# Kernel optimization log

Hardware: AMD Instinct MI355X
Metric: run time of the kernel (lower is better)

The kernel has to match this reference:

```python
import jax, jax.numpy as jnp
import numpy as np

B, L, D = 32, 512, 128
H, D0, D2 = 8, 32, 32
SIGMA = 1.0
NEG = -10000.0


def setup_inputs() -> dict:
    key = jax.random.key(0)
    k_x, k_m, k1, k2, k3, k_w = jax.random.split(key, 6)
    X = jax.random.normal(k_x, (B, L, D), dtype=jnp.float32)
    # random padding mask; guarantee at least one valid item per row
    mask = jax.random.uniform(k_m, (B, L)) < 0.9
    mask = mask.at[:, 0].set(True)
    # nn.Linear(d, H*d0, bias=False): weight shape [H*d0, d], y = x @ W^T
    W1 = SIGMA * jax.random.normal(k1, (H * D0, D), dtype=jnp.float32)
    W2 = SIGMA * jax.random.normal(k2, (H * D0, D), dtype=jnp.float32)
    W3 = SIGMA * jax.random.normal(k3, (H * D2, D), dtype=jnp.float32)
    w = SIGMA * jax.random.normal(k_w, (H, D2), dtype=jnp.float32)
    return {"X": X, "mask": mask, "W1": W1, "W2": W2, "W3": W3, "w": w}


def reference(X, mask, W1, W2, W3, w):
    b, l, d = X.shape
    h, d2 = w.shape
    d0 = W1.shape[0] // h
    Q = (X @ W1.T).reshape(b, l, h, d0)
    K = (X @ W2.T).reshape(b, l, h, d0)
    V = (X @ W3.T).reshape(b, l, h, d2)
    # scores: [B, H, L, L]
    scores = jnp.einsum('blhd,bmhd->bhlm', Q, K) / jnp.sqrt(jnp.asarray(d0, X.dtype))
    # outer-product symmetric pad mask [B,1,L,L]
    am = (mask[:, None, None, :] & mask[:, None, :, None])
    scores = jnp.where(am, scores, jnp.asarray(NEG, X.dtype))
    attn = jax.nn.softmax(scores, axis=-1)
    out = jnp.einsum('bhlm,bmhd->blhd', attn, V)  # [B,L,H,D2]
    v = jnp.einsum('blhd,hd->bl', out, w) / jnp.sqrt(jnp.asarray(h, X.dtype))
    v = jnp.where(mask, v, jnp.asarray(NEG, X.dtype))
    probs = jax.nn.softmax(v, axis=-1)
    return probs
```

## Files before the change

### kernel.cpp

```cpp
#include <hip/hip_runtime.h>
#include <hip/hip_bf16.h>


typedef __attribute__((ext_vector_type(8))) short bf16x8;
typedef __attribute__((ext_vector_type(4))) float f32x4;
typedef __attribute__((ext_vector_type(8))) unsigned short ushort8;
typedef __attribute__((ext_vector_type(4))) unsigned short ushort4v;

#define NEG (-10000.0f)
#define LOG2E 1.4426950408889634f
#define QSCALE (0.17677669529663687f * LOG2E)

__device__ __forceinline__ unsigned short bf16_rn(float x, float* rep) {
  unsigned u = __float_as_uint(x);
  unsigned r = (u + 0x7FFFu + ((u >> 16) & 1u)) >> 16;
  *rep = __uint_as_float(r << 16);
  return (unsigned short)r;
}

__global__ __launch_bounds__(256) void convert_kernel(
    const float* __restrict__ X, const float* __restrict__ W1,
    const float* __restrict__ W2, const float* __restrict__ W3,
    const float* __restrict__ w,
    unsigned short* __restrict__ X2, unsigned short* __restrict__ Wc) {
  const int bx = blockIdx.x, t = threadIdx.x;
  if (bx < 1056) {
    const float* src;
    unsigned short* dst;
    int row, c;
    if (bx < 1024) {
      const size_t flat = (size_t)bx * 2048 + t * 8;
      row = (int)(flat >> 7); c = (int)(flat & 127);
      src = &X[flat];
      dst = &X2[(size_t)row * 256 + c];
    } else {
      const int flat = (bx - 1024) * 2048 + t * 8;
      row = flat >> 7; c = flat & 127;
      src = (row < 256) ? &W1[(size_t)row * 128 + c]
                        : &W2[(size_t)(row - 256) * 128 + c];
      dst = &Wc[(size_t)row * 256 + c];
    }
    float xv[8];
    *(float4*)&xv[0] = *(const float4*)src;
    *(float4*)&xv[4] = *(const float4*)(src + 4);
    ushort8 hi, lo;
#pragma unroll
    for (int i = 0; i < 8; ++i) {
      float hf, lf;
      hi[i] = bf16_rn(xv[i], &hf);
      lo[i] = bf16_rn(xv[i] - hf, &lf);
    }
    *(ushort8*)dst = hi;
    *(ushort8*)(dst + 128) = lo;
  } else {
    __shared__ float uS[8][128];
    if (t < 128) {
#pragma unroll
      for (int h = 0; h < 8; ++h) {
        float acc = 0.f;
#pragma unroll
        for (int d = 0; d < 32; ++d)
          acc += W3[(h * 32 + d) * 128 + t] * w[h * 32 + d];
        uS[h][t] = acc * 0.3535533905932738f;
      }
    }
    __syncthreads();
    {
      const int r = t >> 5, c = (t & 31) * 4;
      float4 v = *(float4*)&uS[r][c];
      float vv[4] = {v.x, v.y, v.z, v.w};
      ushort4v hi, lo;
#pragma unroll
      for (int i = 0; i < 4; ++i) {
        float hf, lf;
        hi[i] = bf16_rn(vv[i], &hf);
        lo[i] = bf16_rn(vv[i] - hf, &lf);
      }
      *(ushort4v*)&Wc[(size_t)(512 + r) * 256 + c] = hi;
      *(ushort4v*)&Wc[(size_t)(512 + r) * 256 + 128 + c] = lo;
    }
    const ushort8 z = {};
    for (int i = t; i < 1792; i += 256)
      *(ushort8*)&Wc[(size_t)520 * 256 + i * 8] = z;
  }
}

__global__ __launch_bounds__(256) void proj_kernel(
    const unsigned short* __restrict__ X2, const unsigned short* __restrict__ Wc,
    unsigned short* __restrict__ Q2, unsigned short* __restrict__ K2,
    float* __restrict__ Vw) {
  __shared__ unsigned short XS[64][72], WSd[64][72], WSx[64][72];
  const int t = threadIdx.x;
  const int row0 = blockIdx.x * 64, col0 = blockIdx.y * 64;
  const int w = t >> 6, lane = t & 63, g = lane >> 4, r16 = lane & 15;
  const int srow = t >> 2, su = (t & 3) * 16;

  f32x4 acc[4];
#pragma unroll
  for (int n = 0; n < 4; ++n) acc[n] = (f32x4){0.f, 0.f, 0.f, 0.f};

  for (int kc = 0; kc < 256; kc += 64) {
    const int kcx = (kc + 128) & 255;
    if (kc) __syncthreads();
    {
      const size_t xo = (size_t)(row0 + srow) * 256 + kc + su;
      const size_t wd = (size_t)(col0 + srow) * 256 + kc + su;
      const size_t wx = (size_t)(col0 + srow) * 256 + kcx + su;
      ushort8 a = *(const ushort8*)&X2[xo];
      ushort8 b = *(const ushort8*)&X2[xo + 8];
      ushort8 c = *(const ushort8*)&Wc[wd];
      ushort8 d = *(const ushort8*)&Wc[wd + 8];
      ushort8 e = *(const ushort8*)&Wc[wx];
      ushort8 f = *(const ushort8*)&Wc[wx + 8];
      *(ushort8*)&XS[srow][su] = a;
      *(ushort8*)&XS[srow][su + 8] = b;
      *(ushort8*)&WSd[srow][su] = c;
      *(ushort8*)&WSd[srow][su + 8] = d;
      *(ushort8*)&WSx[srow][su] = e;
      *(ushort8*)&WSx[srow][su + 8] = f;
    }
    __syncthreads();
#pragma unroll
    for (int ks = 0; ks < 2; ++ks) {
      bf16x8 ah = *(const bf16x8*)&XS[w * 16 + r16][ks * 32 + g * 8];
#pragma unroll
      for (int n = 0; n < 4; ++n) {
        bf16x8 bd = *(const bf16x8*)&WSd[n * 16 + r16][ks * 32 + g * 8];
        bf16x8 bx = *(const bf16x8*)&WSx[n * 16 + r16][ks * 32 + g * 8];
        acc[n] = __builtin_amdgcn_mfma_f32_16x16x32_bf16(ah, bd, acc[n], 0, 0, 0);
        acc[n] = __builtin_amdgcn_mfma_f32_16x16x32_bf16(ah, bx, acc[n], 0, 0, 0);
      }
    }
  }
#pragma unroll
  for (int n = 0; n < 4; ++n) {
    const int col = col0 + n * 16 + r16;
#pragma unroll
    for (int r = 0; r < 4; ++r) {
      const int row = row0 + w * 16 + g * 4 + r;
      const int b = row >> 9, l = row & 511;
      const float val = acc[n][r];
      if (col < 256) {
        const float sv = val * QSCALE;
        float hf, lf;
        const unsigned short hb = bf16_rn(sv, &hf);
        const unsigned short lb = bf16_rn(sv - hf, &lf);
        const size_t o = ((size_t)(b * 8 + (col >> 5)) * 512 + l) * 64 + (col & 31);
        Q2[o] = hb; Q2[o + 32] = lb;
      } else if (col < 512) {
        const int c2 = col - 256;
        float hf, lf;
        const unsigned short hb = bf16_rn(val, &hf);
        const unsigned short lb = bf16_rn(val - hf, &lf);
        const size_t o = ((size_t)(b * 8 + (c2 >> 5)) * 512 + l) * 64 + (c2 & 31);
        K2[o] = hb; K2[o + 32] = lb;
      } else if (col < 520) {
        Vw[(size_t)(b * 8 + (col - 512)) * 512 + l] = val;
      }
    }
  }
}

__global__ __launch_bounds__(512) void attn_kernel(
    const unsigned short* __restrict__ Q2, const unsigned short* __restrict__ K2,
    const float* __restrict__ Vw, const int* __restrict__ mask,
    float* __restrict__ vws) {
  __shared__ unsigned short KS[2][64][72];
  __shared__ float VwS[2][64], biasS[2][64];
  const int t = threadIdx.x;
  const int w = t >> 6, lane = t & 63, g = lane >> 4, r16 = lane & 15;
  const int qbase = blockIdx.x * 256, h = blockIdx.y, b = blockIdx.z;
  const size_t headoff = (size_t)(b * 8 + h) * 512;

  bf16x8 qf[2][2];
#pragma unroll
  for (int qt = 0; qt < 2; ++qt)
#pragma unroll
    for (int ks = 0; ks < 2; ++ks)
      qf[qt][ks] = *(const bf16x8*)
          &Q2[(headoff + qbase + w * 32 + qt * 16 + r16) * 64 + ks * 32 + g * 8];

  const int srow = t >> 3, su = (t & 7) * 8;
  ushort8 kreg = {};
  float vreg = 0.f, breg = 0.f;
  float m[2] = {-1e30f, -1e30f}, lsum[2] = {0.f, 0.f}, val[2] = {0.f, 0.f};

#define LOAD_CH(c)                                                        \
  {                                                                       \
    kreg = *(const ushort8*)&K2[(headoff + (c) * 64 + srow) * 64 + su];   \
    if (t < 64) vreg = Vw[headoff + (c) * 64 + t];                        \
    else if (t < 128)                                                     \
      breg = mask[b * 512 + (c) * 64 + (t - 64)] ? 0.f : NEG * LOG2E;     \
  }
#define WRITE_CH(c)                                                       \
  {                                                                       \
    const int bfi = (c) & 1;                                              \
    *(ushort8*)&KS[bfi][srow][su] = kreg;                                 \
    if (t < 64) VwS[bfi][t] = vreg;                                       \
    else if (t < 128) biasS[bfi][t - 64] = breg;                          \
  }

  LOAD_CH(0);
  WRITE_CH(0);
  __syncthreads();

  for (int c = 0; c < 8; ++c) {
    if (c < 7) LOAD_CH(c + 1);
    const int bfi = c & 1;
    bf16x8 a0[4], a1[4];
#pragma unroll
    for (int j = 0; j < 4; ++j) {
      a0[j] = *(const bf16x8*)&KS[bfi][j * 16 + r16][g * 8];
      a1[j] = *(const bf16x8*)&KS[bfi][j * 16 + r16][32 + g * 8];
    }
    f32x4 sc[4][2];
#pragma unroll
    for (int j = 0; j < 4; ++j)
#pragma unroll
      for (int qt = 0; qt < 2; ++qt) {
        f32x4 z = (f32x4){0.f, 0.f, 0.f, 0.f};
        z = __builtin_amdgcn_mfma_f32_16x16x32_bf16(a0[j], qf[qt][0], z, 0, 0, 0);
        z = __builtin_amdgcn_mfma_f32_16x16x32_bf16(a0[j], qf[qt][1], z, 0, 0, 0);
        z = __builtin_amdgcn_mfma_f32_16x16x32_bf16(a1[j], qf[qt][0], z, 0, 0, 0);
        sc[j][qt] = z;
      }
    float4 bs[4], vw4[4];
#pragma unroll
    for (int j = 0; j < 4; ++j) {
      bs[j]  = *(const float4*)&biasS[bfi][j * 16 + g * 4];
      vw4[j] = *(const float4*)&VwS[bfi][j * 16 + g * 4];
    }
#pragma unroll
    for (int qt = 0; qt < 2; ++qt) {
      float sb[4][4];
      float cmax = -1e30f;
#pragma unroll
      for (int j = 0; j < 4; ++j) {
        sb[j][0] = sc[j][qt][0] + bs[j].x;
        sb[j][1] = sc[j][qt][1] + bs[j].y;
        sb[j][2] = sc[j][qt][2] + bs[j].z;
        sb[j][3] = sc[j][qt][3] + bs[j].w;
#pragma unroll
        for (int r = 0; r < 4; ++r) cmax = fmaxf(cmax, sb[j][r]);
      }
      cmax = fmaxf(cmax, __shfl_xor(cmax, 16));
      cmax = fmaxf(cmax, __shfl_xor(cmax, 32));
      const float mnew = fmaxf(m[qt], cmax);
      const float f = __builtin_amdgcn_exp2f(m[qt] - mnew);
      m[qt] = mnew;
      float ls = lsum[qt] * f, vv = val[qt] * f;
#pragma unroll
      for (int j = 0; j < 4; ++j) {
        const float p0 = __builtin_amdgcn_exp2f(sb[j][0] - mnew);
        const float p1 = __builtin_amdgcn_exp2f(sb[j][1] - mnew);
        const float p2 = __builtin_amdgcn_exp2f(sb[j][2] - mnew);
        const float p3 = __builtin_amdgcn_exp2f(sb[j][3] - mnew);
        ls += (p0 + p1) + (p2 + p3);
        vv = fmaf(p0, vw4[j].x, vv);
        vv = fmaf(p1, vw4[j].y, vv);
        vv = fmaf(p2, vw4[j].z, vv);
        vv = fmaf(p3, vw4[j].w, vv);
      }
      lsum[qt] = ls; val[qt] = vv;
    }
    __syncthreads();
    if (c < 7) {
      WRITE_CH(c + 1);
      __syncthreads();
    }
  }
#pragma unroll
  for (int qt = 0; qt < 2; ++qt) {
    lsum[qt] += __shfl_xor(lsum[qt], 16);
    val[qt]  += __shfl_xor(val[qt], 16);
    lsum[qt] += __shfl_xor(lsum[qt], 32);
    val[qt]  += __shfl_xor(val[qt], 32);
  }
  if (lane < 16) {
#pragma unroll
    for (int qt = 0; qt < 2; ++qt)
      vws[headoff + qbase + w * 32 + qt * 16 + lane] = val[qt] / lsum[qt];
  }
#undef LOAD_CH
#undef WRITE_CH
}

__global__ __launch_bounds__(512) void final_kernel(
    const float* __restrict__ vws, const int* __restrict__ mask,
    float* __restrict__ out) {
  const int b = blockIdx.x, l = threadIdx.x;
  __shared__ float redm[8], reds[8];
  float v = 0.f;
#pragma unroll
  for (int h = 0; h < 8; ++h) v += vws[(size_t)(b * 8 + h) * 512 + l];
  if (mask[b * 512 + l] == 0) v = NEG;
  float mx = v;
#pragma unroll
  for (int off = 32; off >= 1; off >>= 1) mx = fmaxf(mx, __shfl_xor(mx, off));
  if ((l & 63) == 0) redm[l >> 6] = mx;
  __syncthreads();
  float M = redm[0];
#pragma unroll
  for (int i = 1; i < 8; ++i) M = fmaxf(M, redm[i]);
  const float e = __expf(v - M);
  float sm = e;
#pragma unroll
  for (int off = 32; off >= 1; off >>= 1) sm += __shfl_xor(sm, off);
  if ((l & 63) == 0) reds[l >> 6] = sm;
  __syncthreads();
  float S = 0.f;
#pragma unroll
  for (int i = 0; i < 8; ++i) S += reds[i];
  out[b * 512 + l] = e / S;
}

extern "C" void kernel_launch(void* const* d_in, const int* in_sizes, int n_in,
                              void* d_out, int out_size, void* d_ws, size_t ws_size,
                              hipStream_t stream) {
  const float* X  = (const float*)d_in[0];
  const int*  mk  = (const int*)d_in[1];
  const float* W1 = (const float*)d_in[2];
  const float* W2 = (const float*)d_in[3];
  const float* W3 = (const float*)d_in[4];
  const float* w  = (const float*)d_in[5];
  float* out = (float*)d_out;

  char* ws = (char*)d_ws;
  unsigned short* X2 = (unsigned short*)ws;
  unsigned short* Wc = X2 + (size_t)16384 * 256;
  unsigned short* Q2 = Wc + (size_t)576 * 256;
  unsigned short* K2 = Q2 + (size_t)32 * 8 * 512 * 64;
  float* Vw  = (float*)(K2 + (size_t)32 * 8 * 512 * 64);
  float* vws = Vw + (size_t)32 * 8 * 512;

  convert_kernel<<<dim3(1057), dim3(256), 0, stream>>>(X, W1, W2, W3, w, X2, Wc);
  proj_kernel<<<dim3(256, 9), dim3(256), 0, stream>>>(X2, Wc, Q2, K2, Vw);
  attn_kernel<<<dim3(2, 8, 32), dim3(512), 0, stream>>>(Q2, K2, Vw, mk, vws);
  final_kernel<<<dim3(32), dim3(512), 0, stream>>>(vws, mk, out);
}
```

Baseline: 60.25 us.

## Enlarge projection row tile and stage whole K head in LDS for attention

The projection kernel now handles 128 rows per block with two M sub-tiles per wave, so each weight tile loaded into LDS is reused across twice as many rows and the grid is halved. The attention kernel loads the entire 512-row K slice, the Vw values and the mask bias into shared memory once, then drops the double-buffered per-chunk loads and the per-chunk barriers. This cuts global traffic and synchronisation at the cost of much larger LDS use per block (about 76 KB), which may limit how many attention blocks fit on each CU, and the launch bound now asks for four of them.

```diff
diff --git a/kernel.cpp b/kernel.cpp
--- a/kernel.cpp
+++ b/kernel.cpp
@@ -89,46 +89,51 @@
     const unsigned short* __restrict__ X2, const unsigned short* __restrict__ Wc,
     unsigned short* __restrict__ Q2, unsigned short* __restrict__ K2,
     float* __restrict__ Vw) {
-  __shared__ unsigned short XS[64][72], WSd[64][72], WSx[64][72];
+  __shared__ unsigned short XS[128][72], WSd[64][72], WSx[64][72];
   const int t = threadIdx.x;
-  const int row0 = blockIdx.x * 64, col0 = blockIdx.y * 64;
+  const int row0 = blockIdx.x * 128, col0 = blockIdx.y * 64;
   const int w = t >> 6, lane = t & 63, g = lane >> 4, r16 = lane & 15;
-  const int srow = t >> 2, su = (t & 3) * 16;
-
-  f32x4 acc[4];
-#pragma unroll
-  for (int n = 0; n < 4; ++n) acc[n] = (f32x4){0.f, 0.f, 0.f, 0.f};
+
+  f32x4 acc[2][4];
+#pragma unroll
+  for (int mm = 0; mm < 2; ++mm)
+#pragma unroll
+    for (int n = 0; n < 4; ++n) acc[mm][n] = (f32x4){0.f, 0.f, 0.f, 0.f};
 
   for (int kc = 0; kc < 256; kc += 64) {
     const int kcx = (kc + 128) & 255;
     if (kc) __syncthreads();
     {
-      const size_t xo = (size_t)(row0 + srow) * 256 + kc + su;
-      const size_t wd = (size_t)(col0 + srow) * 256 + kc + su;
-      const size_t wx = (size_t)(col0 + srow) * 256 + kcx + su;
-      ushort8 a = *(const ushort8*)&X2[xo];
-      ushort8 b = *(const ushort8*)&X2[xo + 8];
-      ushort8 c = *(const ushort8*)&Wc[wd];
-      ushort8 d = *(const ushort8*)&Wc[wd + 8];
-      ushort8 e = *(const ushort8*)&Wc[wx];
-      ushort8 f = *(const ushort8*)&Wc[wx + 8];
-      *(ushort8*)&XS[srow][su] = a;
-      *(ushort8*)&XS[srow][su + 8] = b;
-      *(ushort8*)&WSd[srow][su] = c;
-      *(ushort8*)&WSd[srow][su + 8] = d;
-      *(ushort8*)&WSx[srow][su] = e;
-      *(ushort8*)&WSx[srow][su + 8] = f;
+#pragma unroll
+      for (int i = 0; i < 4; ++i) {
+        const int flat = i * 256 + t, row = flat >> 3, cg = (flat & 7) * 8;
+        *(ushort8*)&XS[row][cg] =
+            *(const ushort8*)&X2[(size_t)(row0 + row) * 256 + kc + cg];
+      }
+#pragma unroll
+      for (int i = 0; i < 2; ++i) {
+        const int flat = i * 256 + t, row = flat >> 3, cg = (flat & 7) * 8;
+        const size_t wb = (size_t)(col0 + row) * 256;
+        *(ushort8*)&WSd[row][cg] = *(const ushort8*)&Wc[wb + kc + cg];
+        *(ushort8*)&WSx[row][cg] = *(const ushort8*)&Wc[wb + kcx + cg];
+      }
     }
     __syncthreads();
 #pragma unroll
     for (int ks = 0; ks < 2; ++ks) {
-      bf16x8 ah = *(const bf16x8*)&XS[w * 16 + r16][ks * 32 + g * 8];
+      bf16x8 ah[2];
+#pragma unroll
+      for (int mm = 0; mm < 2; ++mm)
+        ah[mm] = *(const bf16x8*)&XS[w * 32 + mm * 16 + r16][ks * 32 + g * 8];
 #pragma unroll
       for (int n = 0; n < 4; ++n) {
         bf16x8 bd = *(const bf16x8*)&WSd[n * 16 + r16][ks * 32 + g * 8];
         bf16x8 bx = *(const bf16x8*)&WSx[n * 16 + r16][ks * 32 + g * 8];
-        acc[n] = __builtin_amdgcn_mfma_f32_16x16x32_bf16(ah, bd, acc[n], 0, 0, 0);
-        acc[n] = __builtin_amdgcn_mfma_f32_16x16x32_bf16(ah, bx, acc[n], 0, 0, 0);
+#pragma unroll
+        for (int mm = 0; mm < 2; ++mm) {
+          acc[mm][n] = __builtin_amdgcn_mfma_f32_16x16x32_bf16(ah[mm], bd, acc[mm][n], 0, 0, 0);
+          acc[mm][n] = __builtin_amdgcn_mfma_f32_16x16x32_bf16(ah[mm], bx, acc[mm][n], 0, 0, 0);
+        }
       }
     }
   }
@@ -136,42 +141,54 @@
   for (int n = 0; n < 4; ++n) {
     const int col = col0 + n * 16 + r16;
 #pragma unroll
-    for (int r = 0; r < 4; ++r) {
-      const int row = row0 + w * 16 + g * 4 + r;
-      const int b = row >> 9, l = row & 511;
-      const float val = acc[n][r];
-      if (col < 256) {
-        const float sv = val * QSCALE;
-        float hf, lf;
-        const unsigned short hb = bf16_rn(sv, &hf);
-        const unsigned short lb = bf16_rn(sv - hf, &lf);
-        const size_t o = ((size_t)(b * 8 + (col >> 5)) * 512 + l) * 64 + (col & 31);
-        Q2[o] = hb; Q2[o + 32] = lb;
-      } else if (col < 512) {
-        const int c2 = col - 256;
-        float hf, lf;
-        const unsigned short hb = bf16_rn(val, &hf);
-        const unsigned short lb = bf16_rn(val - hf, &lf);
-        const size_t o = ((size_t)(b * 8 + (c2 >> 5)) * 512 + l) * 64 + (c2 & 31);
-        K2[o] = hb; K2[o + 32] = lb;
-      } else if (col < 520) {
-        Vw[(size_t)(b * 8 + (col - 512)) * 512 + l] = val;
-      }
-    }
-  }
-}
-
-__global__ __launch_bounds__(512) void attn_kernel(
+    for (int mm = 0; mm < 2; ++mm) {
+#pragma unroll
+      for (int r = 0; r < 4; ++r) {
+        const int row = row0 + w * 32 + mm * 16 + g * 4 + r;
+        const int b = row >> 9, l = row & 511;
+        const float val = acc[mm][n][r];
+        if (col < 256) {
+          const float sv = val * QSCALE;
+          float hf, lf;
+          const unsigned short hb = bf16_rn(sv, &hf);
+          const unsigned short lb = bf16_rn(sv - hf, &lf);
+          const size_t o = ((size_t)(b * 8 + (col >> 5)) * 512 + l) * 64 + (col & 31);
+          Q2[o] = hb; Q2[o + 32] = lb;
+        } else if (col < 512) {
+          const int c2 = col - 256;
+          float hf, lf;
+          const unsigned short hb = bf16_rn(val, &hf);
+          const unsigned short lb = bf16_rn(val - hf, &lf);
+          const size_t o = ((size_t)(b * 8 + (c2 >> 5)) * 512 + l) * 64 + (c2 & 31);
+          K2[o] = hb; K2[o + 32] = lb;
+        } else if (col < 520) {
+          Vw[(size_t)(b * 8 + (col - 512)) * 512 + l] = val;
+        }
+      }
+    }
+  }
+}
+
+__global__ __launch_bounds__(512, 4) void attn_kernel(
     const unsigned short* __restrict__ Q2, const unsigned short* __restrict__ K2,
     const float* __restrict__ Vw, const int* __restrict__ mask,
     float* __restrict__ vws) {
-  __shared__ unsigned short KS[2][64][72];
-  __shared__ float VwS[2][64], biasS[2][64];
+  __shared__ unsigned short KS[512][72];
+  __shared__ float VwS[512], biasS[512];
   const int t = threadIdx.x;
   const int w = t >> 6, lane = t & 63, g = lane >> 4, r16 = lane & 15;
   const int qbase = blockIdx.x * 256, h = blockIdx.y, b = blockIdx.z;
   const size_t headoff = (size_t)(b * 8 + h) * 512;
 
+#pragma unroll
+  for (int i = 0; i < 8; ++i) {
+    const int flat = i * 512 + t;
+    const int row = flat >> 3, cg = (flat & 7) * 8;
+    *(ushort8*)&KS[row][cg] = *(const ushort8*)&K2[(headoff + row) * 64 + cg];
+  }
+  VwS[t] = Vw[headoff + t];
+  biasS[t] = mask[b * 512 + t] ? 0.f : NEG * LOG2E;
+
   bf16x8 qf[2][2];
 #pragma unroll
   for (int qt = 0; qt < 2; ++qt)
@@ -180,38 +197,16 @@
       qf[qt][ks] = *(const bf16x8*)
           &Q2[(headoff + qbase + w * 32 + qt * 16 + r16) * 64 + ks * 32 + g * 8];
 
-  const int srow = t >> 3, su = (t & 7) * 8;
-  ushort8 kreg = {};
-  float vreg = 0.f, breg = 0.f;
+  __syncthreads();
+
   float m[2] = {-1e30f, -1e30f}, lsum[2] = {0.f, 0.f}, val[2] = {0.f, 0.f};
 
-#define LOAD_CH(c)                                                        \
-  {                                                                       \
-    kreg = *(const ushort8*)&K2[(headoff + (c) * 64 + srow) * 64 + su];   \
-    if (t < 64) vreg = Vw[headoff + (c) * 64 + t];                        \
-    else if (t < 128)                                                     \
-      breg = mask[b * 512 + (c) * 64 + (t - 64)] ? 0.f : NEG * LOG2E;     \
-  }
-#define WRITE_CH(c)                                                       \
-  {                                                                       \
-    const int bfi = (c) & 1;                                              \
-    *(ushort8*)&KS[bfi][srow][su] = kreg;                                 \
-    if (t < 64) VwS[bfi][t] = vreg;                                       \
-    else if (t < 128) biasS[bfi][t - 64] = breg;                          \
-  }
-
-  LOAD_CH(0);
-  WRITE_CH(0);
-  __syncthreads();
-
   for (int c = 0; c < 8; ++c) {
-    if (c < 7) LOAD_CH(c + 1);
-    const int bfi = c & 1;
     bf16x8 a0[4], a1[4];
 #pragma unroll
     for (int j = 0; j < 4; ++j) {
-      a0[j] = *(const bf16x8*)&KS[bfi][j * 16 + r16][g * 8];
-      a1[j] = *(const bf16x8*)&KS[bfi][j * 16 + r16][32 + g * 8];
+      a0[j] = *(const bf16x8*)&KS[c * 64 + j * 16 + r16][g * 8];
+      a1[j] = *(const bf16x8*)&KS[c * 64 + j * 16 + r16][32 + g * 8];
     }
     f32x4 sc[4][2];
 #pragma unroll
@@ -224,22 +219,17 @@
         z = __builtin_amdgcn_mfma_f32_16x16x32_bf16(a1[j], qf[qt][0], z, 0, 0, 0);
         sc[j][qt] = z;
       }
-    float4 bs[4], vw4[4];
-#pragma unroll
-    for (int j = 0; j < 4; ++j) {
-      bs[j]  = *(const float4*)&biasS[bfi][j * 16 + g * 4];
-      vw4[j] = *(const float4*)&VwS[bfi][j * 16 + g * 4];
-    }
 #pragma unroll
     for (int qt = 0; qt < 2; ++qt) {
       float sb[4][4];
       float cmax = -1e30f;
 #pragma unroll
       for (int j = 0; j < 4; ++j) {
-        sb[j][0] = sc[j][qt][0] + bs[j].x;
-        sb[j][1] = sc[j][qt][1] + bs[j].y;
-        sb[j][2] = sc[j][qt][2] + bs[j].z;
-        sb[j][3] = sc[j][qt][3] + bs[j].w;
+        const float4 bsj = *(const float4*)&biasS[c * 64 + j * 16 + g * 4];
+        sb[j][0] = sc[j][qt][0] + bsj.x;
+        sb[j][1] = sc[j][qt][1] + bsj.y;
+        sb[j][2] = sc[j][qt][2] + bsj.z;
+        sb[j][3] = sc[j][qt][3] + bsj.w;
 #pragma unroll
         for (int r = 0; r < 4; ++r) cmax = fmaxf(cmax, sb[j][r]);
       }
@@ -251,22 +241,18 @@
       float ls = lsum[qt] * f, vv = val[qt] * f;
 #pragma unroll
       for (int j = 0; j < 4; ++j) {
+        const float4 vwj = *(const float4*)&VwS[c * 64 + j * 16 + g * 4];
         const float p0 = __builtin_amdgcn_exp2f(sb[j][0] - mnew);
         const float p1 = __builtin_amdgcn_exp2f(sb[j][1] - mnew);
         const float p2 = __builtin_amdgcn_exp2f(sb[j][2] - mnew);
         const float p3 = __builtin_amdgcn_exp2f(sb[j][3] - mnew);
         ls += (p0 + p1) + (p2 + p3);
-        vv = fmaf(p0, vw4[j].x, vv);
-        vv = fmaf(p1, vw4[j].y, vv);
-        vv = fmaf(p2, vw4[j].z, vv);
-        vv = fmaf(p3, vw4[j].w, vv);
+        vv = fmaf(p0, vwj.x, vv);
+        vv = fmaf(p1, vwj.y, vv);
+        vv = fmaf(p2, vwj.z, vv);
+        vv = fmaf(p3, vwj.w, vv);
       }
       lsum[qt] = ls; val[qt] = vv;
-    }
-    __syncthreads();
-    if (c < 7) {
-      WRITE_CH(c + 1);
-      __syncthreads();
     }
   }
 #pragma unroll
@@ -281,8 +267,6 @@
     for (int qt = 0; qt < 2; ++qt)
       vws[headoff + qbase + w * 32 + qt * 16 + lane] = val[qt] / lsum[qt];
   }
-#undef LOAD_CH
-#undef WRITE_CH
 }
 
 __global__ __launch_bounds__(512) void final_kernel(
@@ -334,7 +318,7 @@
   float* vws = Vw + (size_t)32 * 8 * 512;
 
   convert_kernel<<<dim3(1057), dim3(256), 0, stream>>>(X, W1, W2, W3, w, X2, Wc);
-  proj_kernel<<<dim3(256, 9), dim3(256), 0, stream>>>(X2, Wc, Q2, K2, Vw);
+  proj_kernel<<<dim3(128, 9), dim3(256), 0, stream>>>(X2, Wc, Q2, K2, Vw);
   attn_kernel<<<dim3(2, 8, 32), dim3(512), 0, stream>>>(Q2, K2, Vw, mk, vws);
   final_kernel<<<dim3(32), dim3(512), 0, stream>>>(vws, mk, out);
 }
```

Measured after the change: 62.24 us. 1.03x slower.

## Split attention over key chunks per wave with separate combine kernel

Applied to the files above, without the earlier changes.

The attention kernel is restructured so that each wave handles one 16-query tile against one 128-key slice. K, mask and Vw are read directly from global memory instead of being staged through double-buffered shared memory with block barriers. Partial max, sum and value results go to workspace and a new combine kernel merges the four key slices with a log-sum-exp rescale. This exposes far more parallel work and removes the shared-memory syncs. The cost is an extra kernel launch, extra partial-result traffic, and K tiles re-read from global memory by each query tile rather than shared within a block.

```diff
diff --git a/kernel.cpp b/kernel.cpp
--- a/kernel.cpp
+++ b/kernel.cpp
@@ -10,6 +10,7 @@
 #define NEG (-10000.0f)
 #define LOG2E 1.4426950408889634f
 #define QSCALE (0.17677669529663687f * LOG2E)
+#define NEGL (NEG * LOG2E)
 
 __device__ __forceinline__ unsigned short bf16_rn(float x, float* rep) {
   unsigned u = __float_as_uint(x);
@@ -161,128 +162,109 @@
   }
 }
 
-__global__ __launch_bounds__(512) void attn_kernel(
+__global__ __launch_bounds__(256) void attn_kernel(
     const unsigned short* __restrict__ Q2, const unsigned short* __restrict__ K2,
     const float* __restrict__ Vw, const int* __restrict__ mask,
-    float* __restrict__ vws) {
-  __shared__ unsigned short KS[2][64][72];
-  __shared__ float VwS[2][64], biasS[2][64];
-  const int t = threadIdx.x;
-  const int w = t >> 6, lane = t & 63, g = lane >> 4, r16 = lane & 15;
-  const int qbase = blockIdx.x * 256, h = blockIdx.y, b = blockIdx.z;
-  const size_t headoff = (size_t)(b * 8 + h) * 512;
-
-  bf16x8 qf[2][2];
-#pragma unroll
-  for (int qt = 0; qt < 2; ++qt)
-#pragma unroll
-    for (int ks = 0; ks < 2; ++ks)
-      qf[qt][ks] = *(const bf16x8*)
-          &Q2[(headoff + qbase + w * 32 + qt * 16 + r16) * 64 + ks * 32 + g * 8];
-
-  const int srow = t >> 3, su = (t & 7) * 8;
-  ushort8 kreg = {};
-  float vreg = 0.f, breg = 0.f;
-  float m[2] = {-1e30f, -1e30f}, lsum[2] = {0.f, 0.f}, val[2] = {0.f, 0.f};
-
-#define LOAD_CH(c)                                                        \
-  {                                                                       \
-    kreg = *(const ushort8*)&K2[(headoff + (c) * 64 + srow) * 64 + su];   \
-    if (t < 64) vreg = Vw[headoff + (c) * 64 + t];                        \
-    else if (t < 128)                                                     \
-      breg = mask[b * 512 + (c) * 64 + (t - 64)] ? 0.f : NEG * LOG2E;     \
-  }
-#define WRITE_CH(c)                                                       \
-  {                                                                       \
-    const int bfi = (c) & 1;                                              \
-    *(ushort8*)&KS[bfi][srow][su] = kreg;                                 \
-    if (t < 64) VwS[bfi][t] = vreg;                                       \
-    else if (t < 128) biasS[bfi][t - 64] = breg;                          \
-  }
-
-  LOAD_CH(0);
-  WRITE_CH(0);
-  __syncthreads();
-
-  for (int c = 0; c < 8; ++c) {
-    if (c < 7) LOAD_CH(c + 1);
-    const int bfi = c & 1;
+    float* __restrict__ Pm, float* __restrict__ Pl, float* __restrict__ Pv) {
+  const int lane = threadIdx.x & 63;
+  const int g = lane >> 4, r16 = lane & 15;
+  const int task = blockIdx.x * 4 + (threadIdx.x >> 6);
+  const int ks = task & 3;
+  const int qt = (task >> 2) & 31;
+  const int head = task >> 7;
+  const int b = head >> 3;
+  const size_t headoff = (size_t)head * 512;
+
+  const size_t qrow = headoff + qt * 16 + r16;
+  const bf16x8 qh = *(const bf16x8*)&Q2[qrow * 64 + g * 8];
+  const bf16x8 ql = *(const bf16x8*)&Q2[qrow * 64 + 32 + g * 8];
+
+  float m = -1e30f, lsum = 0.f, val = 0.f;
+
+#pragma unroll
+  for (int cc = 0; cc < 2; ++cc) {
+    const int key0 = ks * 128 + cc * 64;
     bf16x8 a0[4], a1[4];
+    int4 mk4[4];
+    float4 vw4[4];
 #pragma unroll
     for (int j = 0; j < 4; ++j) {
-      a0[j] = *(const bf16x8*)&KS[bfi][j * 16 + r16][g * 8];
-      a1[j] = *(const bf16x8*)&KS[bfi][j * 16 + r16][32 + g * 8];
-    }
-    f32x4 sc[4][2];
-#pragma unroll
-    for (int j = 0; j < 4; ++j)
-#pragma unroll
-      for (int qt = 0; qt < 2; ++qt) {
-        f32x4 z = (f32x4){0.f, 0.f, 0.f, 0.f};
-        z = __builtin_amdgcn_mfma_f32_16x16x32_bf16(a0[j], qf[qt][0], z, 0, 0, 0);
-        z = __builtin_amdgcn_mfma_f32_16x16x32_bf16(a0[j], qf[qt][1], z, 0, 0, 0);
-        z = __builtin_amdgcn_mfma_f32_16x16x32_bf16(a1[j], qf[qt][0], z, 0, 0, 0);
-        sc[j][qt] = z;
-      }
-    float4 bs[4], vw4[4];
+      const size_t krow = headoff + key0 + j * 16 + r16;
+      a0[j] = *(const bf16x8*)&K2[krow * 64 + g * 8];
+      a1[j] = *(const bf16x8*)&K2[krow * 64 + 32 + g * 8];
+      mk4[j] = *(const int4*)&mask[b * 512 + key0 + j * 16 + g * 4];
+      vw4[j] = *(const float4*)&Vw[headoff + key0 + j * 16 + g * 4];
+    }
+    f32x4 sc[4];
 #pragma unroll
     for (int j = 0; j < 4; ++j) {
-      bs[j]  = *(const float4*)&biasS[bfi][j * 16 + g * 4];
-      vw4[j] = *(const float4*)&VwS[bfi][j * 16 + g * 4];
-    }
-#pragma unroll
-    for (int qt = 0; qt < 2; ++qt) {
-      float sb[4][4];
-      float cmax = -1e30f;
-#pragma unroll
-      for (int j = 0; j < 4; ++j) {
-        sb[j][0] = sc[j][qt][0] + bs[j].x;
-        sb[j][1] = sc[j][qt][1] + bs[j].y;
-        sb[j][2] = sc[j][qt][2] + bs[j].z;
-        sb[j][3] = sc[j][qt][3] + bs[j].w;
-#pragma unroll
-        for (int r = 0; r < 4; ++r) cmax = fmaxf(cmax, sb[j][r]);
-      }
-      cmax = fmaxf(cmax, __shfl_xor(cmax, 16));
-      cmax = fmaxf(cmax, __shfl_xor(cmax, 32));
-      const float mnew = fmaxf(m[qt], cmax);
-      const float f = __builtin_amdgcn_exp2f(m[qt] - mnew);
-      m[qt] = mnew;
-      float ls = lsum[qt] * f, vv = val[qt] * f;
-#pragma unroll
-      for (int j = 0; j < 4; ++j) {
-        const float p0 = __builtin_amdgcn_exp2f(sb[j][0] - mnew);
-        const float p1 = __builtin_amdgcn_exp2f(sb[j][1] - mnew);
-        const float p2 = __builtin_amdgcn_exp2f(sb[j][2] - mnew);
-        const float p3 = __builtin_amdgcn_exp2f(sb[j][3] - mnew);
-        ls += (p0 + p1) + (p2 + p3);
-        vv = fmaf(p0, vw4[j].x, vv);
-        vv = fmaf(p1, vw4[j].y, vv);
-        vv = fmaf(p2, vw4[j].z, vv);
-        vv = fmaf(p3, vw4[j].w, vv);
-      }
-      lsum[qt] = ls; val[qt] = vv;
-    }
-    __syncthreads();
-    if (c < 7) {
-      WRITE_CH(c + 1);
-      __syncthreads();
-    }
-  }
-#pragma unroll
-  for (int qt = 0; qt < 2; ++qt) {
-    lsum[qt] += __shfl_xor(lsum[qt], 16);
-    val[qt]  += __shfl_xor(val[qt], 16);
-    lsum[qt] += __shfl_xor(lsum[qt], 32);
-    val[qt]  += __shfl_xor(val[qt], 32);
-  }
+      f32x4 z = (f32x4){0.f, 0.f, 0.f, 0.f};
+      z = __builtin_amdgcn_mfma_f32_16x16x32_bf16(a0[j], qh, z, 0, 0, 0);
+      z = __builtin_amdgcn_mfma_f32_16x16x32_bf16(a0[j], ql, z, 0, 0, 0);
+      z = __builtin_amdgcn_mfma_f32_16x16x32_bf16(a1[j], qh, z, 0, 0, 0);
+      sc[j] = z;
+    }
+    float sb[4][4];
+    float cmax = -1e30f;
+#pragma unroll
+    for (int j = 0; j < 4; ++j) {
+      sb[j][0] = sc[j][0] + (mk4[j].x ? 0.f : NEGL);
+      sb[j][1] = sc[j][1] + (mk4[j].y ? 0.f : NEGL);
+      sb[j][2] = sc[j][2] + (mk4[j].z ? 0.f : NEGL);
+      sb[j][3] = sc[j][3] + (mk4[j].w ? 0.f : NEGL);
+#pragma unroll
+      for (int r = 0; r < 4; ++r) cmax = fmaxf(cmax, sb[j][r]);
+    }
+    cmax = fmaxf(cmax, __shfl_xor(cmax, 16));
+    cmax = fmaxf(cmax, __shfl_xor(cmax, 32));
+    const float mnew = fmaxf(m, cmax);
+    const float f = __builtin_amdgcn_exp2f(m - mnew);
+    m = mnew;
+    float ls = lsum * f, vv = val * f;
+#pragma unroll
+    for (int j = 0; j < 4; ++j) {
+      const float p0 = __builtin_amdgcn_exp2f(sb[j][0] - mnew);
+      const float p1 = __builtin_amdgcn_exp2f(sb[j][1] - mnew);
+      const float p2 = __builtin_amdgcn_exp2f(sb[j][2] - mnew);
+      const float p3 = __builtin_amdgcn_exp2f(sb[j][3] - mnew);
+      ls += (p0 + p1) + (p2 + p3);
+      vv = fmaf(p0, vw4[j].x, vv);
+      vv = fmaf(p1, vw4[j].y, vv);
+      vv = fmaf(p2, vw4[j].z, vv);
+      vv = fmaf(p3, vw4[j].w, vv);
+    }
+    lsum = ls; val = vv;
+  }
+  lsum += __shfl_xor(lsum, 16);
+  val  += __shfl_xor(val, 16);
+  lsum += __shfl_xor(lsum, 32);
+  val  += __shfl_xor(val, 32);
   if (lane < 16) {
-#pragma unroll
-    for (int qt = 0; qt < 2; ++qt)
-      vws[headoff + qbase + w * 32 + qt * 16 + lane] = val[qt] / lsum[qt];
-  }
-#undef LOAD_CH
-#undef WRITE_CH
+    const size_t po = (size_t)task * 16 + r16;
+    Pm[po] = m; Pl[po] = lsum; Pv[po] = val;
+  }
+}
+
+__global__ __launch_bounds__(256) void combine_kernel(
+    const float* __restrict__ Pm, const float* __restrict__ Pl,
+    const float* __restrict__ Pv, float* __restrict__ vws) {
+  const int i = blockIdx.x * 256 + threadIdx.x;
+  const int q16 = i & 15, tile = i >> 4;
+  float m[4], l[4], v[4];
+#pragma unroll
+  for (int s = 0; s < 4; ++s) {
+    const size_t po = ((size_t)tile * 4 + s) * 16 + q16;
+    m[s] = Pm[po]; l[s] = Pl[po]; v[s] = Pv[po];
+  }
+  const float ms = fmaxf(fmaxf(m[0], m[1]), fmaxf(m[2], m[3]));
+  float L = 0.f, V = 0.f;
+#pragma unroll
+  for (int s = 0; s < 4; ++s) {
+    const float f = __builtin_amdgcn_exp2f(m[s] - ms);
+    L = fmaf(l[s], f, L);
+    V = fmaf(v[s], f, V);
+  }
+  vws[i] = V / L;
 }
 
 __global__ __launch_bounds__(512) void final_kernel(
@@ -332,9 +314,13 @@
   unsigned short* K2 = Q2 + (size_t)32 * 8 * 512 * 64;
   float* Vw  = (float*)(K2 + (size_t)32 * 8 * 512 * 64);
   float* vws = Vw + (size_t)32 * 8 * 512;
+  float* Pm  = vws + (size_t)32 * 8 * 512;
+  float* Pl  = Pm + (size_t)32768 * 16;
+  float* Pv  = Pl + (size_t)32768 * 16;
 
   convert_kernel<<<dim3(1057), dim3(256), 0, stream>>>(X, W1, W2, W3, w, X2, Wc);
   proj_kernel<<<dim3(256, 9), dim3(256), 0, stream>>>(X2, Wc, Q2, K2, Vw);
-  attn_kernel<<<dim3(2, 8, 32), dim3(512), 0, stream>>>(Q2, K2, Vw, mk, vws);
+  attn_kernel<<<dim3(8192), dim3(256), 0, stream>>>(Q2, K2, Vw, mk, Pm, Pl, Pv);
+  combine_kernel<<<dim3(512), dim3(256), 0, stream>>>(Pm, Pl, Pv, vws);
   final_kernel<<<dim3(32), dim3(512), 0, stream>>>(vws, mk, out);
 }
```

New measurement: 115.4 us. +91.5%, slower.

## Stage proj epilogue through LDS and use two-pass softmax over full K

Applied to the files above, without the earlier changes.

The projection epilogue now stages accumulators in shared memory so each thread writes contiguous 16-byte vectors of Q/K hi/lo parts instead of scattered 2-byte stores. The grid is also transposed so the column tiles of one row block launch adjacently, which should improve reuse of X in cache. The attention kernel loads the whole head's K, Vw and mask bias into LDS once and replaces the online softmax with two passes: one to find the max and one to accumulate exp sums. This removes the per-chunk barriers and rescaling, but it recomputes the QK MFMAs and needs about 78KB of LDS per block, which may limit occupancy.

```diff
diff --git a/kernel.cpp b/kernel.cpp
--- a/kernel.cpp
+++ b/kernel.cpp
@@ -90,8 +90,9 @@
     unsigned short* __restrict__ Q2, unsigned short* __restrict__ K2,
     float* __restrict__ Vw) {
   __shared__ unsigned short XS[64][72], WSd[64][72], WSx[64][72];
+  __shared__ float SOUT[64][68];
   const int t = threadIdx.x;
-  const int row0 = blockIdx.x * 64, col0 = blockIdx.y * 64;
+  const int row0 = blockIdx.y * 64, col0 = blockIdx.x * 64;
   const int w = t >> 6, lane = t & 63, g = lane >> 4, r16 = lane & 15;
   const int srow = t >> 2, su = (t & 3) * 16;
 
@@ -132,31 +133,51 @@
       }
     }
   }
-#pragma unroll
-  for (int n = 0; n < 4; ++n) {
-    const int col = col0 + n * 16 + r16;
-#pragma unroll
-    for (int r = 0; r < 4; ++r) {
-      const int row = row0 + w * 16 + g * 4 + r;
-      const int b = row >> 9, l = row & 511;
-      const float val = acc[n][r];
-      if (col < 256) {
-        const float sv = val * QSCALE;
+  __syncthreads();
+#pragma unroll
+  for (int n = 0; n < 4; ++n)
+#pragma unroll
+    for (int r = 0; r < 4; ++r)
+      SOUT[w * 16 + g * 4 + r][n * 16 + r16] = acc[n][r];
+  __syncthreads();
+  {
+    const int row = t >> 2, q4 = t & 3;
+    const int grow = row0 + row, bb = grow >> 9, l = grow & 511;
+    const int gc0 = col0 + q4 * 16;
+    float v16[16];
+#pragma unroll
+    for (int i = 0; i < 4; ++i)
+      *(float4*)&v16[i * 4] = *(float4*)&SOUT[row][q4 * 16 + i * 4];
+    if (gc0 < 512) {
+      const bool isQ = gc0 < 256;
+      const int c2 = isQ ? gc0 : gc0 - 256;
+      const int head = c2 >> 5, d0 = c2 & 31;
+      const float scl = isQ ? QSCALE : 1.f;
+      ushort8 hi0, hi1, lo0, lo1;
+#pragma unroll
+      for (int i = 0; i < 8; ++i) {
         float hf, lf;
-        const unsigned short hb = bf16_rn(sv, &hf);
-        const unsigned short lb = bf16_rn(sv - hf, &lf);
-        const size_t o = ((size_t)(b * 8 + (col >> 5)) * 512 + l) * 64 + (col & 31);
-        Q2[o] = hb; Q2[o + 32] = lb;
-      } else if (col < 512) {
-        const int c2 = col - 256;
+        const float sv = v16[i] * scl;
+        hi0[i] = bf16_rn(sv, &hf);
+        lo0[i] = bf16_rn(sv - hf, &lf);
+      }
+#pragma unroll
+      for (int i = 0; i < 8; ++i) {
         float hf, lf;
-        const unsigned short hb = bf16_rn(val, &hf);
-        const unsigned short lb = bf16_rn(val - hf, &lf);
-        const size_t o = ((size_t)(b * 8 + (c2 >> 5)) * 512 + l) * 64 + (c2 & 31);
-        K2[o] = hb; K2[o + 32] = lb;
-      } else if (col < 520) {
-        Vw[(size_t)(b * 8 + (col - 512)) * 512 + l] = val;
-      }
+        const float sv = v16[8 + i] * scl;
+        hi1[i] = bf16_rn(sv, &hf);
+        lo1[i] = bf16_rn(sv - hf, &lf);
+      }
+      unsigned short* dst =
+          (isQ ? Q2 : K2) + ((size_t)(bb * 8 + head) * 512 + l) * 64 + d0;
+      *(ushort8*)dst = hi0;
+      *(ushort8*)(dst + 8) = hi1;
+      *(ushort8*)(dst + 32) = lo0;
+      *(ushort8*)(dst + 40) = lo1;
+    } else if (gc0 < 520) {
+#pragma unroll
+      for (int i = 0; i < 8; ++i)
+        Vw[(size_t)(bb * 8 + i) * 512 + l] = v16[i];
     }
   }
 }
@@ -165,13 +186,21 @@
     const unsigned short* __restrict__ Q2, const unsigned short* __restrict__ K2,
     const float* __restrict__ Vw, const int* __restrict__ mask,
     float* __restrict__ vws) {
-  __shared__ unsigned short KS[2][64][72];
-  __shared__ float VwS[2][64], biasS[2][64];
+  __shared__ unsigned short KS[512][72];
+  __shared__ float VwS[512], biasS[512];
   const int t = threadIdx.x;
   const int w = t >> 6, lane = t & 63, g = lane >> 4, r16 = lane & 15;
   const int qbase = blockIdx.x * 256, h = blockIdx.y, b = blockIdx.z;
   const size_t headoff = (size_t)(b * 8 + h) * 512;
 
+#pragma unroll
+  for (int i = 0; i < 8; ++i) {
+    const int flat = i * 512 + t, row = flat >> 3, cg = (flat & 7) * 8;
+    *(ushort8*)&KS[row][cg] = *(const ushort8*)&K2[(headoff + row) * 64 + cg];
+  }
+  VwS[t] = Vw[headoff + t];
+  biasS[t] = mask[b * 512 + t] ? 0.f : NEG * LOG2E;
+
   bf16x8 qf[2][2];
 #pragma unroll
   for (int qt = 0; qt < 2; ++qt)
@@ -180,109 +209,79 @@
       qf[qt][ks] = *(const bf16x8*)
           &Q2[(headoff + qbase + w * 32 + qt * 16 + r16) * 64 + ks * 32 + g * 8];
 
-  const int srow = t >> 3, su = (t & 7) * 8;
-  ushort8 kreg = {};
-  float vreg = 0.f, breg = 0.f;
-  float m[2] = {-1e30f, -1e30f}, lsum[2] = {0.f, 0.f}, val[2] = {0.f, 0.f};
-
-#define LOAD_CH(c)                                                        \
-  {                                                                       \
-    kreg = *(const ushort8*)&K2[(headoff + (c) * 64 + srow) * 64 + su];   \
-    if (t < 64) vreg = Vw[headoff + (c) * 64 + t];                        \
-    else if (t < 128)                                                     \
-      breg = mask[b * 512 + (c) * 64 + (t - 64)] ? 0.f : NEG * LOG2E;     \
-  }
-#define WRITE_CH(c)                                                       \
-  {                                                                       \
-    const int bfi = (c) & 1;                                              \
-    *(ushort8*)&KS[bfi][srow][su] = kreg;                                 \
-    if (t < 64) VwS[bfi][t] = vreg;                                       \
-    else if (t < 128) biasS[bfi][t - 64] = breg;                          \
-  }
-
-  LOAD_CH(0);
-  WRITE_CH(0);
-  __syncthreads();
-
+  __syncthreads();
+
+  float mx[2] = {-3e38f, -3e38f};
   for (int c = 0; c < 8; ++c) {
-    if (c < 7) LOAD_CH(c + 1);
-    const int bfi = c & 1;
     bf16x8 a0[4], a1[4];
 #pragma unroll
     for (int j = 0; j < 4; ++j) {
-      a0[j] = *(const bf16x8*)&KS[bfi][j * 16 + r16][g * 8];
-      a1[j] = *(const bf16x8*)&KS[bfi][j * 16 + r16][32 + g * 8];
-    }
-    f32x4 sc[4][2];
-#pragma unroll
-    for (int j = 0; j < 4; ++j)
-#pragma unroll
-      for (int qt = 0; qt < 2; ++qt) {
+      a0[j] = *(const bf16x8*)&KS[c * 64 + j * 16 + r16][g * 8];
+      a1[j] = *(const bf16x8*)&KS[c * 64 + j * 16 + r16][32 + g * 8];
+    }
+#pragma unroll
+    for (int qt = 0; qt < 2; ++qt) {
+#pragma unroll
+      for (int j = 0; j < 4; ++j) {
         f32x4 z = (f32x4){0.f, 0.f, 0.f, 0.f};
         z = __builtin_amdgcn_mfma_f32_16x16x32_bf16(a0[j], qf[qt][0], z, 0, 0, 0);
         z = __builtin_amdgcn_mfma_f32_16x16x32_bf16(a0[j], qf[qt][1], z, 0, 0, 0);
         z = __builtin_amdgcn_mfma_f32_16x16x32_bf16(a1[j], qf[qt][0], z, 0, 0, 0);
-        sc[j][qt] = z;
-      }
-    float4 bs[4], vw4[4];
+        const float4 bsj = *(const float4*)&biasS[c * 64 + j * 16 + g * 4];
+        const float m01 = fmaxf(z[0] + bsj.x, z[1] + bsj.y);
+        const float m23 = fmaxf(z[2] + bsj.z, z[3] + bsj.w);
+        mx[qt] = fmaxf(mx[qt], fmaxf(m01, m23));
+      }
+    }
+  }
+#pragma unroll
+  for (int qt = 0; qt < 2; ++qt) {
+    mx[qt] = fmaxf(mx[qt], __shfl_xor(mx[qt], 16));
+    mx[qt] = fmaxf(mx[qt], __shfl_xor(mx[qt], 32));
+  }
+
+  float ls[2] = {0.f, 0.f}, vv[2] = {0.f, 0.f};
+  for (int c = 0; c < 8; ++c) {
+    bf16x8 a0[4], a1[4];
 #pragma unroll
     for (int j = 0; j < 4; ++j) {
-      bs[j]  = *(const float4*)&biasS[bfi][j * 16 + g * 4];
-      vw4[j] = *(const float4*)&VwS[bfi][j * 16 + g * 4];
+      a0[j] = *(const bf16x8*)&KS[c * 64 + j * 16 + r16][g * 8];
+      a1[j] = *(const bf16x8*)&KS[c * 64 + j * 16 + r16][32 + g * 8];
     }
 #pragma unroll
     for (int qt = 0; qt < 2; ++qt) {
-      float sb[4][4];
-      float cmax = -1e30f;
 #pragma unroll
       for (int j = 0; j < 4; ++j) {
-        sb[j][0] = sc[j][qt][0] + bs[j].x;
-        sb[j][1] = sc[j][qt][1] + bs[j].y;
-        sb[j][2] = sc[j][qt][2] + bs[j].z;
-        sb[j][3] = sc[j][qt][3] + bs[j].w;
-#pragma unroll
-        for (int r = 0; r < 4; ++r) cmax = fmaxf(cmax, sb[j][r]);
-      }
-      cmax = fmaxf(cmax, __shfl_xor(cmax, 16));
-      cmax = fmaxf(cmax, __shfl_xor(cmax, 32));
-      const float mnew = fmaxf(m[qt], cmax);
-      const float f = __builtin_amdgcn_exp2f(m[qt] - mnew);
-      m[qt] = mnew;
-      float ls = lsum[qt] * f, vv = val[qt] * f;
-#pragma unroll
-      for (int j = 0; j < 4; ++j) {
-        const float p0 = __builtin_amdgcn_exp2f(sb[j][0] - mnew);
-        const float p1 = __builtin_amdgcn_exp2f(sb[j][1] - mnew);
-        const float p2 = __builtin_amdgcn_exp2f(sb[j][2] - mnew);
-        const float p3 = __builtin_amdgcn_exp2f(sb[j][3] - mnew);
-        ls += (p0 + p1) + (p2 + p3);
-        vv = fmaf(p0, vw4[j].x, vv);
-        vv = fmaf(p1, vw4[j].y, vv);
-        vv = fmaf(p2, vw4[j].z, vv);
-        vv = fmaf(p3, vw4[j].w, vv);
-      }
-      lsum[qt] = ls; val[qt] = vv;
-    }
-    __syncthreads();
-    if (c < 7) {
-      WRITE_CH(c + 1);
-      __syncthreads();
+        f32x4 z = (f32x4){0.f, 0.f, 0.f, 0.f};
+        z = __builtin_amdgcn_mfma_f32_16x16x32_bf16(a0[j], qf[qt][0], z, 0, 0, 0);
+        z = __builtin_amdgcn_mfma_f32_16x16x32_bf16(a0[j], qf[qt][1], z, 0, 0, 0);
+        z = __builtin_amdgcn_mfma_f32_16x16x32_bf16(a1[j], qf[qt][0], z, 0, 0, 0);
+        const float4 bsj = *(const float4*)&biasS[c * 64 + j * 16 + g * 4];
+        const float4 vwj = *(const float4*)&VwS[c * 64 + j * 16 + g * 4];
+        const float p0 = __builtin_amdgcn_exp2f(z[0] + bsj.x - mx[qt]);
+        const float p1 = __builtin_amdgcn_exp2f(z[1] + bsj.y - mx[qt]);
+        const float p2 = __builtin_amdgcn_exp2f(z[2] + bsj.z - mx[qt]);
+        const float p3 = __builtin_amdgcn_exp2f(z[3] + bsj.w - mx[qt]);
+        ls[qt] += (p0 + p1) + (p2 + p3);
+        float a = fmaf(p0, vwj.x, vv[qt]);
+        a = fmaf(p1, vwj.y, a);
+        a = fmaf(p2, vwj.z, a);
+        vv[qt] = fmaf(p3, vwj.w, a);
+      }
     }
   }
 #pragma unroll
   for (int qt = 0; qt < 2; ++qt) {
-    lsum[qt] += __shfl_xor(lsum[qt], 16);
-    val[qt]  += __shfl_xor(val[qt], 16);
-    lsum[qt] += __shfl_xor(lsum[qt], 32);
-    val[qt]  += __shfl_xor(val[qt], 32);
+    ls[qt] += __shfl_xor(ls[qt], 16);
+    vv[qt] += __shfl_xor(vv[qt], 16);
+    ls[qt] += __shfl_xor(ls[qt], 32);
+    vv[qt] += __shfl_xor(vv[qt], 32);
   }
   if (lane < 16) {
 #pragma unroll
     for (int qt = 0; qt < 2; ++qt)
-      vws[headoff + qbase + w * 32 + qt * 16 + lane] = val[qt] / lsum[qt];
-  }
-#undef LOAD_CH
-#undef WRITE_CH
+      vws[headoff + qbase + w * 32 + qt * 16 + lane] = vv[qt] / ls[qt];
+  }
 }
 
 __global__ __launch_bounds__(512) void final_kernel(
@@ -334,7 +333,7 @@
   float* vws = Vw + (size_t)32 * 8 * 512;
 
   convert_kernel<<<dim3(1057), dim3(256), 0, stream>>>(X, W1, W2, W3, w, X2, Wc);
-  proj_kernel<<<dim3(256, 9), dim3(256), 0, stream>>>(X2, Wc, Q2, K2, Vw);
+  proj_kernel<<<dim3(9, 256), dim3(256), 0, stream>>>(X2, Wc, Q2, K2, Vw);
   attn_kernel<<<dim3(2, 8, 32), dim3(512), 0, stream>>>(Q2, K2, Vw, mk, vws);
   final_kernel<<<dim3(32), dim3(512), 0, stream>>>(vws, mk, out);
 }
```

Result: slower. 72.98 us (+21.1%).
